# Kernel optimization log

Measured on AMD Instinct MI355X. Metric: run time of the kernel, lower is better.

Reference implementation:

```python
import jax, jax.numpy as jnp
import numpy as np

BATCH, IN_F, OUT_F, K = 16384, 1024, 1024, 256


def setup_inputs() -> dict:
    key = jax.random.key(0)
    kx, kw, kp = jax.random.split(key, 3)
    x = jax.random.normal(kx, (BATCH, IN_F), dtype=jnp.float32)
    weights = jax.random.normal(kw, (OUT_F, IN_F), dtype=jnp.float32)
    P = jax.random.normal(kp, (K, IN_F), dtype=jnp.float32)  # LSH projection matrix (K, in_features)
    return {"x": x, "weights": weights, "P": P}


def _codes(unit, P):
    # SimHash binary codes in {-1, +1}: sign of random projections
    return jnp.where(unit @ P.T >= 0, 1.0, -1.0).astype(unit.dtype)


def reference(x, weights, P):
    eps = jnp.finfo(x.dtype).eps
    # normalize rows of x and weights
    x_norms = jnp.linalg.norm(x, axis=-1, keepdims=True) + eps        # (B, 1)
    x_unit = x / x_norms
    w_norms = jnp.linalg.norm(weights, axis=-1, keepdims=True) + eps  # (M, 1)
    w_unit = weights / w_norms
    # hash codes
    codes_x = _codes(x_unit, P)   # (B, K)
    codes_w = _codes(w_unit, P)   # (M, K)
    # agreement-based cosine estimate: dot/K = 1 - 2*hamming_frac
    dot = codes_x @ codes_w.T                                   # (B, M)
    k = jnp.asarray(P.shape[0], dtype=x.dtype)
    half_pi = jnp.asarray(np.pi * 0.5, dtype=x.dtype)
    cos_est = jnp.cos(half_pi * (1.0 - dot / k))                # (B, M)
    return x_norms * w_norms.T * cos_est                        # (B, M)
```

## Files before the change

### kernel.cpp

```cpp
#include <hip/hip_runtime.h>
#include <math.h>

#define BATCH 16384
#define OUTF  1024
#define INF   1024
#define KPROJ 256
#define MTOT  (BATCH + OUTF)

#define NZ_THRESH 0.15f

typedef unsigned long long u64;
typedef unsigned short     u16;
typedef _Float16           f16;
typedef __attribute__((ext_vector_type(8))) _Float16 f16x8;
typedef __attribute__((ext_vector_type(4))) float    f32x4;

#define SCHED0() __builtin_amdgcn_sched_barrier(0)

__global__ __launch_bounds__(256) void prep_p(const float* __restrict__ P,
                                              f16* __restrict__ Bf) {
    const int c = blockIdx.x;
    const int p = threadIdx.x;
    const float4 f0 = *(const float4*)(P + (size_t)p * INF + c * 8);
    const float4 f1 = *(const float4*)(P + (size_t)p * INF + c * 8 + 4);
    const int kt = c >> 3, ks = (c >> 2) & 1, lq = c & 3;
    const int frag = (kt * 16 + (p >> 4)) * 2 + ks;
    const int lane = lq * 16 + (p & 15);
    f16x8 h;
    h[0] = (f16)f0.x; h[1] = (f16)f0.y; h[2] = (f16)f0.z; h[3] = (f16)f0.w;
    h[4] = (f16)f1.x; h[5] = (f16)f1.y; h[6] = (f16)f1.z; h[7] = (f16)f1.w;
    *(f16x8*)(Bf + (size_t)(frag * 64 + lane) * 8) = h;
}

__global__ __launch_bounds__(256, 2) void gemm_signs(const float* __restrict__ X,
                                                     const float* __restrict__ W,
                                                     const f16* __restrict__ Bf,
                                                     const float* __restrict__ Pf,
                                                     u64* __restrict__ cx,
                                                     u64* __restrict__ cw,
                                                     float* __restrict__ xn,
                                                     float* __restrict__ wn) {
    __shared__ f32x4 red[2][16][64];
    __shared__ float nsq[4][16];
    __shared__ u16 sw[16][16];

    const int t    = threadIdx.x;
    const int wid  = t >> 6, lane = t & 63;
    const int l4   = lane >> 4, l15 = lane & 15;
    const int row0 = blockIdx.x * 16;
    const int kb   = ((wid + blockIdx.x) & 3) * 4;
    const int roff = (blockIdx.x * 5) & 15;

    const float* Asrc = (row0 < BATCH) ? X + (size_t)row0 * INF
                                       : W + (size_t)(row0 - BATCH) * INF;
    const float* aPtr = Asrc + (size_t)l15 * INF + l4 * 8;

    f16x8 af[8];
    float ssq = 0.0f;
#pragma unroll
    for (int i = 0; i < 4; ++i) {
        const float* p = aPtr + (kb + i) * 64;
        float4 q0 = *(const float4*)(p);
        float4 q1 = *(const float4*)(p + 4);
        float4 q2 = *(const float4*)(p + 32);
        float4 q3 = *(const float4*)(p + 36);
        ssq += q0.x * q0.x + q0.y * q0.y + q0.z * q0.z + q0.w * q0.w +
               q1.x * q1.x + q1.y * q1.y + q1.z * q1.z + q1.w * q1.w +
               q2.x * q2.x + q2.y * q2.y + q2.z * q2.z + q2.w * q2.w +
               q3.x * q3.x + q3.y * q3.y + q3.z * q3.z + q3.w * q3.w;
        f16x8 a0, a1;
        a0[0] = (f16)q0.x; a0[1] = (f16)q0.y; a0[2] = (f16)q0.z; a0[3] = (f16)q0.w;
        a0[4] = (f16)q1.x; a0[5] = (f16)q1.y; a0[6] = (f16)q1.z; a0[7] = (f16)q1.w;
        a1[0] = (f16)q2.x; a1[1] = (f16)q2.y; a1[2] = (f16)q2.z; a1[3] = (f16)q2.w;
        a1[4] = (f16)q3.x; a1[5] = (f16)q3.y; a1[6] = (f16)q3.z; a1[7] = (f16)q3.w;
        af[2 * i]     = a0;
        af[2 * i + 1] = a1;
    }

    int joff[16];
#pragma unroll
    for (int s = 0; s < 16; ++s) joff[s] = ((s + roff) & 15) * 1024;

    f32x4 acc[16] = {};
    const f16* bq = Bf + lane * 8;

    f16x8 bA0, bA1, bA2, bA3, bA4, bA5, bA6, bA7;
    f16x8 bB0, bB1, bB2, bB3, bB4, bB5, bB6, bB7;
    f16x8 bC0, bC1, bC2, bC3, bC4, bC5, bC6, bC7;

#define BLOAD(BUF, G)                                                         \
    {                                                                         \
        const f16* bt_ = bq + (size_t)(kb + ((G) >> 2)) * 16384;              \
        BUF##0 = *(const f16x8*)(bt_ + joff[((G) & 3) * 4 + 0]);              \
        BUF##1 = *(const f16x8*)(bt_ + joff[((G) & 3) * 4 + 0] + 512);        \
        BUF##2 = *(const f16x8*)(bt_ + joff[((G) & 3) * 4 + 1]);              \
        BUF##3 = *(const f16x8*)(bt_ + joff[((G) & 3) * 4 + 1] + 512);        \
        BUF##4 = *(const f16x8*)(bt_ + joff[((G) & 3) * 4 + 2]);              \
        BUF##5 = *(const f16x8*)(bt_ + joff[((G) & 3) * 4 + 2] + 512);        \
        BUF##6 = *(const f16x8*)(bt_ + joff[((G) & 3) * 4 + 3]);              \
        BUF##7 = *(const f16x8*)(bt_ + joff[((G) & 3) * 4 + 3] + 512);        \
    }

#define BMFMA(BUF, G)                                                         \
    {                                                                         \
        acc[((G) & 3) * 4 + 0] = __builtin_amdgcn_mfma_f32_16x16x32_f16(      \
            af[2 * ((G) >> 2)],     BUF##0, acc[((G) & 3) * 4 + 0], 0, 0, 0); \
        acc[((G) & 3) * 4 + 0] = __builtin_amdgcn_mfma_f32_16x16x32_f16(      \
            af[2 * ((G) >> 2) + 1], BUF##1, acc[((G) & 3) * 4 + 0], 0, 0, 0); \
        acc[((G) & 3) * 4 + 1] = __builtin_amdgcn_mfma_f32_16x16x32_f16(      \
            af[2 * ((G) >> 2)],     BUF##2, acc[((G) & 3) * 4 + 1], 0, 0, 0); \
        acc[((G) & 3) * 4 + 1] = __builtin_amdgcn_mfma_f32_16x16x32_f16(      \
            af[2 * ((G) >> 2) + 1], BUF##3, acc[((G) & 3) * 4 + 1], 0, 0, 0); \
        acc[((G) & 3) * 4 + 2] = __builtin_amdgcn_mfma_f32_16x16x32_f16(      \
            af[2 * ((G) >> 2)],     BUF##4, acc[((G) & 3) * 4 + 2], 0, 0, 0); \
        acc[((G) & 3) * 4 + 2] = __builtin_amdgcn_mfma_f32_16x16x32_f16(      \
            af[2 * ((G) >> 2) + 1], BUF##5, acc[((G) & 3) * 4 + 2], 0, 0, 0); \
        acc[((G) & 3) * 4 + 3] = __builtin_amdgcn_mfma_f32_16x16x32_f16(      \
            af[2 * ((G) >> 2)],     BUF##6, acc[((G) & 3) * 4 + 3], 0, 0, 0); \
        acc[((G) & 3) * 4 + 3] = __builtin_amdgcn_mfma_f32_16x16x32_f16(      \
            af[2 * ((G) >> 2) + 1], BUF##7, acc[((G) & 3) * 4 + 3], 0, 0, 0); \
    }

#define STEPL(BUF, G, VM, GN)                                                 \
    asm volatile("s_waitcnt vmcnt(" VM ")" ::: "memory");                     \
    SCHED0();                                                                 \
    BMFMA(BUF, G);                                                            \
    BLOAD(BUF, GN);                                                           \
    SCHED0();

#define STEPN(BUF, G, VM)                                                     \
    asm volatile("s_waitcnt vmcnt(" VM ")" ::: "memory");                     \
    SCHED0();                                                                 \
    BMFMA(BUF, G);                                                            \
    SCHED0();

    BLOAD(bA, 0);
    BLOAD(bB, 1);
    BLOAD(bC, 2);
    STEPL(bA, 0,  "16", 3);
    STEPL(bB, 1,  "16", 4);
    STEPL(bC, 2,  "16", 5);
    STEPL(bA, 3,  "16", 6);
    STEPL(bB, 4,  "16", 7);
    STEPL(bC, 5,  "16", 8);
    STEPL(bA, 6,  "16", 9);
    STEPL(bB, 7,  "16", 10);
    STEPL(bC, 8,  "16", 11);
    STEPL(bA, 9,  "16", 12);
    STEPL(bB, 10, "16", 13);
    STEPL(bC, 11, "16", 14);
    STEPL(bA, 12, "16", 15);
    STEPN(bB, 13, "16");
    STEPN(bC, 14, "8");
    STEPN(bA, 15, "0");

    ssq += __shfl_xor(ssq, 16, 64);
    ssq += __shfl_xor(ssq, 32, 64);
    if (lane < 16) nsq[wid][l15] = ssq;

    if (wid == 1)
#pragma unroll
        for (int j = 0; j < 16; ++j) red[0][j][lane] = acc[j];
    if (wid == 3)
#pragma unroll
        for (int j = 0; j < 16; ++j) red[1][j][lane] = acc[j];
    __syncthreads();
    if (wid == 0)
#pragma unroll
        for (int j = 0; j < 16; ++j) acc[j] += red[0][j][lane];
    if (wid == 2)
#pragma unroll
        for (int j = 0; j < 16; ++j) {
            acc[j] += red[1][j][lane];
            red[1][j][lane] = acc[j];
        }
    if (wid == 1 && lane < 16) {
        const float s = nsq[0][lane] + nsq[1][lane] + nsq[2][lane] + nsq[3][lane];
        const float n = sqrtf(s) + 1.1920929e-07f;
        const int grow = row0 + lane;
        if (grow < BATCH) xn[grow] = n; else wn[grow - BATCH] = n;
    }
    __syncthreads();
    if (wid == 0)
#pragma unroll
        for (int j = 0; j < 16; ++j) {
            acc[j] += red[1][j][lane];
            red[0][j][lane] = acc[j];
        }
    __syncthreads();

    f32x4 facc[4];
#pragma unroll
    for (int jj = 0; jj < 4; ++jj) facc[jj] = red[0][wid * 4 + jj][lane];

#pragma unroll
    for (int jj = 0; jj < 4; ++jj) {
        const int j = (wid * 4 + jj + roff) & 15;
#pragma unroll
        for (int q = 0; q < 4; ++q) {
            const float v = facc[jj][q];
            int bit = (v >= 0.0f) ? 1 : 0;
            u64 fl = __ballot(fabsf(v) < NZ_THRESH);
            while (fl) {
                const int src = __ffsll((long long)fl) - 1;
                fl &= fl - 1;
                const int lrow = ((src >> 4) << 2) + q;
                const int col  = j * 16 + (src & 15);
                const float* xr = Asrc + (size_t)lrow * INF + lane * 16;
                const float* pr = Pf + (size_t)col * INF + lane * 16;
                double s = 0.0;
#pragma unroll
                for (int c4 = 0; c4 < 4; ++c4) {
                    float4 xa = *(const float4*)(xr + c4 * 4);
                    float4 pa = *(const float4*)(pr + c4 * 4);
                    s += (double)xa.x * pa.x + (double)xa.y * pa.y +
                         (double)xa.z * pa.z + (double)xa.w * pa.w;
                }
#pragma unroll
                for (int off = 32; off; off >>= 1) s += __shfl_xor(s, off, 64);
                if (lane == src) bit = (s >= 0.0) ? 1 : 0;
            }
            const u64 b = __ballot(bit != 0);
            if (l15 == 0)
                sw[l4 * 4 + q][j] = (u16)(b >> (l4 * 16));
        }
    }
    __syncthreads();
    if (t < 64) {
        const int r = t >> 2, w = t & 3;
        const u64 val = *(const u64*)&sw[r][w * 4];
        const int grow = row0 + r;
        if (grow < BATCH) cx[(size_t)grow * 4 + w] = val;
        else              cw[(size_t)(grow - BATCH) * 4 + w] = val;
    }
}

__global__ __launch_bounds__(256) void popc_out(const u64* __restrict__ cx,
                                                const u64* __restrict__ cw,
                                                const float* __restrict__ xn,
                                                const float* __restrict__ wn,
                                                float* __restrict__ out) {
    __shared__ float lut[257];
    __shared__ u64 cxs[64][4];
    __shared__ float xns[64];
    const int t = threadIdx.x;

    lut[t] = (float)cos((double)t * (3.14159265358979323846 / 256.0));
    if (t == 0) lut[256] = -1.0f;

    const int r0 = blockIdx.x * 64;
    cxs[t >> 2][t & 3] = cx[(size_t)r0 * 4 + t];
    if (t < 64) xns[t] = xn[r0 + t];

    const ulonglong4* cwv4 = (const ulonglong4*)cw;
    ulonglong4 c0 = cwv4[4 * t + 0];
    ulonglong4 c1 = cwv4[4 * t + 1];
    ulonglong4 c2 = cwv4[4 * t + 2];
    ulonglong4 c3 = cwv4[4 * t + 3];
    float4 wnr = ((const float4*)wn)[t];

    __syncthreads();

    float4* outv = (float4*)out;
    const size_t obase = (size_t)r0 * (OUTF / 4) + t;
#pragma unroll 4
    for (int r = 0; r < 64; ++r) {
        const u64 a0 = cxs[r][0], a1 = cxs[r][1], a2 = cxs[r][2], a3 = cxs[r][3];
        const float sx = xns[r];
        float4 o;
        o.x = sx * wnr.x * lut[__popcll(a0 ^ c0.x) + __popcll(a1 ^ c0.y) +
                               __popcll(a2 ^ c0.z) + __popcll(a3 ^ c0.w)];
        o.y = sx * wnr.y * lut[__popcll(a0 ^ c1.x) + __popcll(a1 ^ c1.y) +
                               __popcll(a2 ^ c1.z) + __popcll(a3 ^ c1.w)];
        o.z = sx * wnr.z * lut[__popcll(a0 ^ c2.x) + __popcll(a1 ^ c2.y) +
                               __popcll(a2 ^ c2.z) + __popcll(a3 ^ c2.w)];
        o.w = sx * wnr.w * lut[__popcll(a0 ^ c3.x) + __popcll(a1 ^ c3.y) +
                               __popcll(a2 ^ c3.z) + __popcll(a3 ^ c3.w)];
        outv[obase + (size_t)r * (OUTF / 4)] = o;
    }
}

extern "C" void kernel_launch(void* const* d_in, const int* in_sizes, int n_in,
                              void* d_out, int out_size, void* d_ws, size_t ws_size,
                              hipStream_t stream) {
    const float* x = (const float*)d_in[0];
    const float* w = (const float*)d_in[1];
    const float* P = (const float*)d_in[2];
    float* out = (float*)d_out;

    char* ws = (char*)d_ws;
    f16*  Bf = (f16*)ws;
    u64*  cx = (u64*)(ws + 524288);
    u64*  cw = (u64*)(ws + 1048576);
    float* xn = (float*)(ws + 1081344);
    float* wn = (float*)(ws + 1146880);

    prep_p<<<128, 256, 0, stream>>>(P, Bf);

    gemm_signs<<<MTOT / 16, 256, 0, stream>>>(x, w, Bf, P, cx, cw, xn, wn);

    popc_out<<<BATCH / 64, 256, 0, stream>>>(cx, cw, xn, wn, out);
}
```

Baseline: 75.95 us.

## Defer near-zero sign recomputation to a separate queued fixup kernel

Instead of recomputing ambiguous projections in fp64 inline inside the sign GEMM, which serialises one wave per flagged element and diverges, flagged entries are appended to a global queue with an atomic counter. A new fixup kernel then recomputes them in parallel and flips the affected code bits with atomicXor. The P preparation kernel is restructured to stage rows through shared memory, and the GEMM's occupancy hint is raised to 4 blocks per CU. This adds a kernel launch and a memset, and the queue is capped, so any overflow beyond the cap is silently left uncorrected.

```diff
diff --git a/kernel.cpp b/kernel.cpp
--- a/kernel.cpp
+++ b/kernel.cpp
@@ -8,7 +8,9 @@
 #define MTOT  (BATCH + OUTF)
 
 #define NZ_THRESH 0.15f
-
+#define QCAP 49152u
+
+typedef unsigned int       u32;
 typedef unsigned long long u64;
 typedef unsigned short     u16;
 typedef _Float16           f16;
@@ -19,27 +21,36 @@
 
 __global__ __launch_bounds__(256) void prep_p(const float* __restrict__ P,
                                               f16* __restrict__ Bf) {
-    const int c = blockIdx.x;
-    const int p = threadIdx.x;
-    const float4 f0 = *(const float4*)(P + (size_t)p * INF + c * 8);
-    const float4 f1 = *(const float4*)(P + (size_t)p * INF + c * 8 + 4);
-    const int kt = c >> 3, ks = (c >> 2) & 1, lq = c & 3;
-    const int frag = (kt * 16 + (p >> 4)) * 2 + ks;
-    const int lane = lq * 16 + (p & 15);
-    f16x8 h;
-    h[0] = (f16)f0.x; h[1] = (f16)f0.y; h[2] = (f16)f0.z; h[3] = (f16)f0.w;
-    h[4] = (f16)f1.x; h[5] = (f16)f1.y; h[6] = (f16)f1.z; h[7] = (f16)f1.w;
-    *(f16x8*)(Bf + (size_t)(frag * 64 + lane) * 8) = h;
-}
-
-__global__ __launch_bounds__(256, 2) void gemm_signs(const float* __restrict__ X,
+    __shared__ f16 tile[16][1024];
+    const int j = blockIdx.x;
+    const int t = threadIdx.x;
+#pragma unroll
+    for (int r = 0; r < 16; ++r) {
+        const float4 f = ((const float4*)(P + (size_t)(j * 16 + r) * INF))[t];
+        f16* d = &tile[r][t * 4];
+        d[0] = (f16)f.x; d[1] = (f16)f.y; d[2] = (f16)f.z; d[3] = (f16)f.w;
+    }
+    __syncthreads();
+    const int lane = t & 63, fo = t >> 6;
+    const int lq = lane >> 4, l15 = lane & 15;
+#pragma unroll
+    for (int g = 0; g < 8; ++g) {
+        const int f  = g * 4 + fo;
+        const int kt = f >> 1, ks = f & 1;
+        f16x8 h = *(const f16x8*)&tile[l15][kt * 64 + ks * 32 + lq * 8];
+        *(f16x8*)(Bf + (size_t)((((kt * 16 + j) * 2 + ks) * 64) + lane) * 8) = h;
+    }
+}
+
+__global__ __launch_bounds__(256, 4) void gemm_signs(const float* __restrict__ X,
                                                      const float* __restrict__ W,
                                                      const f16* __restrict__ Bf,
-                                                     const float* __restrict__ Pf,
                                                      u64* __restrict__ cx,
                                                      u64* __restrict__ cw,
                                                      float* __restrict__ xn,
-                                                     float* __restrict__ wn) {
+                                                     float* __restrict__ wn,
+                                                     u32* __restrict__ cnt,
+                                                     u32* __restrict__ queue) {
     __shared__ f32x4 red[2][16][64];
     __shared__ float nsq[4][16];
     __shared__ u16 sw[16][16];
@@ -199,26 +210,19 @@
 #pragma unroll
         for (int q = 0; q < 4; ++q) {
             const float v = facc[jj][q];
-            int bit = (v >= 0.0f) ? 1 : 0;
-            u64 fl = __ballot(fabsf(v) < NZ_THRESH);
-            while (fl) {
-                const int src = __ffsll((long long)fl) - 1;
-                fl &= fl - 1;
-                const int lrow = ((src >> 4) << 2) + q;
-                const int col  = j * 16 + (src & 15);
-                const float* xr = Asrc + (size_t)lrow * INF + lane * 16;
-                const float* pr = Pf + (size_t)col * INF + lane * 16;
-                double s = 0.0;
-#pragma unroll
-                for (int c4 = 0; c4 < 4; ++c4) {
-                    float4 xa = *(const float4*)(xr + c4 * 4);
-                    float4 pa = *(const float4*)(pr + c4 * 4);
-                    s += (double)xa.x * pa.x + (double)xa.y * pa.y +
-                         (double)xa.z * pa.z + (double)xa.w * pa.w;
+            const int bit = (v >= 0.0f) ? 1 : 0;
+            const u64 fl = __ballot(fabsf(v) < NZ_THRESH);
+            if (fl) {
+                u32 base;
+                if (lane == 0) base = atomicAdd(cnt, (u32)__popcll(fl));
+                base = (u32)__shfl((int)base, 0, 64);
+                if ((fl >> lane) & 1ull) {
+                    const u32 rank = (u32)__popcll(fl & ((1ull << lane) - 1ull));
+                    const u32 idx  = base + rank;
+                    const u32 grow = (u32)(row0 + l4 * 4 + q);
+                    const u32 col  = (u32)(j * 16 + l15);
+                    if (idx < QCAP) queue[idx] = (grow << 9) | (col << 1) | (u32)bit;
                 }
-#pragma unroll
-                for (int off = 32; off; off >>= 1) s += __shfl_xor(s, off, 64);
-                if (lane == src) bit = (s >= 0.0) ? 1 : 0;
             }
             const u64 b = __ballot(bit != 0);
             if (l15 == 0)
@@ -232,6 +236,45 @@
         const int grow = row0 + r;
         if (grow < BATCH) cx[(size_t)grow * 4 + w] = val;
         else              cw[(size_t)(grow - BATCH) * 4 + w] = val;
+    }
+}
+
+__global__ __launch_bounds__(256) void fixup_k(const float* __restrict__ X,
+                                               const float* __restrict__ W,
+                                               const float* __restrict__ Pf,
+                                               u64* __restrict__ cx,
+                                               u64* __restrict__ cw,
+                                               const u32* __restrict__ cnt,
+                                               const u32* __restrict__ queue) {
+    const int lane = threadIdx.x & 63;
+    const u32 gw = blockIdx.x * 4 + (threadIdx.x >> 6);
+    const u32 nw = gridDim.x * 4;
+    const u32 n0 = *cnt;
+    const u32 n  = (n0 < QCAP) ? n0 : QCAP;
+    for (u32 it = gw; it < n; it += nw) {
+        const u32 v    = queue[it];
+        const u32 row  = v >> 9;
+        const u32 col  = (v >> 1) & 255u;
+        const u32 obit = v & 1u;
+        const float* xr = ((row < BATCH) ? X + (size_t)row * INF
+                                         : W + (size_t)(row - BATCH) * INF) + lane * 16;
+        const float* pr = Pf + (size_t)col * INF + lane * 16;
+        double s = 0.0;
+#pragma unroll
+        for (int c4 = 0; c4 < 4; ++c4) {
+            float4 xa = *(const float4*)(xr + c4 * 4);
+            float4 pa = *(const float4*)(pr + c4 * 4);
+            s += (double)xa.x * pa.x + (double)xa.y * pa.y +
+                 (double)xa.z * pa.z + (double)xa.w * pa.w;
+        }
+#pragma unroll
+        for (int off = 32; off; off >>= 1) s += __shfl_xor(s, off, 64);
+        const u32 nbit = (s >= 0.0) ? 1u : 0u;
+        if (lane == 0 && nbit != obit) {
+            u64* wptr = (row < BATCH) ? &cx[(size_t)row * 4 + (col >> 6)]
+                                      : &cw[(size_t)(row - BATCH) * 4 + (col >> 6)];
+            atomicXor(wptr, 1ull << (col & 63));
+        }
     }
 }
 
@@ -289,15 +332,20 @@
     float* out = (float*)d_out;
 
     char* ws = (char*)d_ws;
-    f16*  Bf = (f16*)ws;
+    f16*  Bp = (f16*)ws;
     u64*  cx = (u64*)(ws + 524288);
     u64*  cw = (u64*)(ws + 1048576);
     float* xn = (float*)(ws + 1081344);
     float* wn = (float*)(ws + 1146880);
-
-    prep_p<<<128, 256, 0, stream>>>(P, Bf);
-
-    gemm_signs<<<MTOT / 16, 256, 0, stream>>>(x, w, Bf, P, cx, cw, xn, wn);
+    u32*  cnt = (u32*)(ws + 1150976);
+    u32*  qu  = (u32*)(ws + 1151232);
+
+    prep_p<<<16, 256, 0, stream>>>(P, Bp);
+    hipMemsetAsync(cnt, 0, 4, stream);
+
+    gemm_signs<<<MTOT / 16, 256, 0, stream>>>(x, w, Bp, cx, cw, xn, wn, cnt, qu);
+
+    fixup_k<<<512, 256, 0, stream>>>(x, w, P, cx, cw, cnt, qu);
 
     popc_out<<<BATCH / 64, 256, 0, stream>>>(cx, cw, xn, wn, out);
 }
```

New measurement: 298.9 us. 3.94x slower.
